# Kernel tuning notes

Hardware: AMD Instinct MI355X
Metric: run time of the kernel (lower is better)

Reference implementation:

```python
import jax, jax.numpy as jnp
import numpy as np
import math

N, S, D, H, L, F = 4, 2048, 512, 8, 4, 200
HD = D // H
EPS = 1e-5


def _pos_encoding(seq_len, d_model, dtype):
    pos = jnp.arange(seq_len, dtype=jnp.float32)[:, None]            # [S,1]
    div = jnp.exp(jnp.arange(0, d_model, 2, dtype=jnp.float32) * (-math.log(10000.0) / d_model))
    ang = pos * div                                                   # [S,D/2]
    pe = jnp.stack([jnp.sin(ang), jnp.cos(ang)], axis=-1).reshape(seq_len, d_model)
    return pe.astype(dtype)


def _layernorm(x, w, b):
    mu = jnp.mean(x, axis=-1, keepdims=True)
    var = jnp.mean(jnp.square(x - mu), axis=-1, keepdims=True)
    return (x - mu) * jax.lax.rsqrt(var + EPS) * w + b


def setup_inputs() -> dict:
    key = jax.random.key(0)
    ks = jax.random.split(key, 8)
    std = 0.02
    inp = {
        "features": jax.random.normal(ks[0], (N, S, D), dtype=jnp.float32),
        # attention projections, stored as [L, in, out] (math-equivalent to torch x @ W.T + b)
        "Wq": jax.random.normal(ks[1], (L, D, D), dtype=jnp.float32) * std,
        "bq": jnp.zeros((L, D), dtype=jnp.float32),
        "Wk": jax.random.normal(ks[2], (L, D, D), dtype=jnp.float32) * std,
        "bk": jnp.zeros((L, D), dtype=jnp.float32),
        "Wv": jax.random.normal(ks[3], (L, D, D), dtype=jnp.float32) * std,
        "bv": jnp.zeros((L, D), dtype=jnp.float32),
        "Wo": jax.random.normal(ks[4], (L, D, D), dtype=jnp.float32) * std,
        "bo": jnp.zeros((L, D), dtype=jnp.float32),
        # FFN
        "W1": jax.random.normal(ks[5], (L, D, F), dtype=jnp.float32) * std,
        "b1": jnp.zeros((L, F), dtype=jnp.float32),
        "W2": jax.random.normal(ks[6], (L, F, D), dtype=jnp.float32) * std,
        "b2": jnp.zeros((L, D), dtype=jnp.float32),
        # layernorms
        "ln1_w": jnp.ones((L, D), dtype=jnp.float32),
        "ln1_b": jnp.zeros((L, D), dtype=jnp.float32),
        "ln2_w": jnp.ones((L, D), dtype=jnp.float32),
        "ln2_b": jnp.zeros((L, D), dtype=jnp.float32),
    }
    return inp


def _encoder(features, Wq, bq, Wk, bk, Wv, bv, Wo, bo, W1, b1, W2, b2,
             ln1_w, ln1_b, ln2_w, ln2_b):
    n, s, d = features.shape
    x = features + _pos_encoding(s, d, features.dtype)[None]  # PositionalEncoding (dropout=identity in eval)
    scale = 1.0 / math.sqrt(HD)
    for l in range(L):
        # MultiHeadAttention: manual QK^T -> softmax -> AV
        q = (x @ Wq[l] + bq[l]).reshape(n, s, H, HD)
        k = (x @ Wk[l] + bk[l]).reshape(n, s, H, HD)
        v = (x @ Wv[l] + bv[l]).reshape(n, s, H, HD)
        attn = jnp.einsum("nshd,nthd->nhst", q, k) * scale          # [N,H,S,S]
        score = jax.nn.softmax(attn, axis=-1)
        y = jnp.einsum("nhst,nthd->nshd", score, v).reshape(n, s, d)
        attn_out = y @ Wo[l] + bo[l]
        x = _layernorm(x + attn_out, ln1_w[l], ln1_b[l])
        # FFN: linear2(relu(linear1(x)))
        ff = jax.nn.relu(x @ W1[l] + b1[l]) @ W2[l] + b2[l]
        x = _layernorm(x + ff, ln2_w[l], ln2_b[l])
    return x


def reference(features, Wq, bq, Wk, bk, Wv, bv, Wo, bo, W1, b1, W2, b2,
              ln1_w, ln1_b, ln2_w, ln2_b):
    return _encoder(features, Wq, bq, Wk, bk, Wv, bv, Wo, bo, W1, b1, W2, b2,
                    ln1_w, ln1_b, ln2_w, ln2_b)
```

## Files before the change

### kernel.cpp

```cpp
#include <hip/hip_runtime.h>
#include <hip/hip_bf16.h>
#include <cstdint>


typedef __bf16 bf16;
typedef __bf16 bf16x8 __attribute__((ext_vector_type(8)));
typedef float f32x4 __attribute__((ext_vector_type(4)));

#define MFMA16(a, b, c) __builtin_amdgcn_mfma_f32_16x16x32_bf16((a), (b), (c), 0, 0, 0)

static constexpr int NB   = 4;
static constexpr int SQ   = 2048;
static constexpr int DM   = 512;
static constexpr int NH   = 8;
static constexpr int HD   = 64;
static constexpr int NL   = 4;
static constexpr int FF   = 200;
static constexpr int FFP  = 256;
static constexpr int MTOK = NB * SQ;

__device__ __forceinline__ float fast_exp2(float x) {
#if __has_builtin(__builtin_amdgcn_exp2f)
    return __builtin_amdgcn_exp2f(x);
#else
    return exp2f(x);
#endif
}

__device__ __forceinline__ void gld16(bf16* l, const bf16* g) {
    __builtin_amdgcn_global_load_lds(
        (const __attribute__((address_space(1))) void*)g,
        (__attribute__((address_space(3))) void*)l, 16, 0, 0);
}

__global__ __launch_bounds__(256) void convw_kernel(
    const float* __restrict__ Wq, const float* __restrict__ Wk,
    const float* __restrict__ Wv, const float* __restrict__ Wo,
    const float* __restrict__ W1, const float* __restrict__ W2,
    bf16* __restrict__ wqkvt, bf16* __restrict__ wot,
    bf16* __restrict__ w1t, bf16* __restrict__ w2t)
{
    __shared__ float tile[32][33];
    const int z = blockIdx.z, l = z / 6, which = z % 6;
    const float* src; bf16* dst; int K, Nsrc, Npad, Kpad;
    switch (which) {
        case 0: src = Wq + (size_t)l*DM*DM; dst = wqkvt + (size_t)(l*3+0)*DM*DM; K=DM; Nsrc=DM; Npad=DM; Kpad=DM; break;
        case 1: src = Wk + (size_t)l*DM*DM; dst = wqkvt + (size_t)(l*3+1)*DM*DM; K=DM; Nsrc=DM; Npad=DM; Kpad=DM; break;
        case 2: src = Wv + (size_t)l*DM*DM; dst = wqkvt + (size_t)(l*3+2)*DM*DM; K=DM; Nsrc=DM; Npad=DM; Kpad=DM; break;
        case 3: src = Wo + (size_t)l*DM*DM; dst = wot   + (size_t)l*DM*DM;       K=DM; Nsrc=DM; Npad=DM; Kpad=DM; break;
        case 4: src = W1 + (size_t)l*DM*FF; dst = w1t   + (size_t)l*FFP*DM;      K=DM; Nsrc=FF; Npad=FFP; Kpad=DM; break;
        default:src = W2 + (size_t)l*FF*DM; dst = w2t   + (size_t)l*DM*FFP;      K=FF; Nsrc=DM; Npad=DM; Kpad=FFP; break;
    }
    const int k0 = blockIdx.x * 32, n0 = blockIdx.y * 32;
    if (k0 >= Kpad || n0 >= Npad) return;
    const int tr = threadIdx.x >> 3, tc = (threadIdx.x & 7) * 4;
    for (int c = 0; c < 4; c++) {
        int sr = k0 + tr, sc = n0 + tc + c;
        tile[tr][tc + c] = (sr < K && sc < Nsrc) ? src[(size_t)sr * Nsrc + sc] : 0.f;
    }
    __syncthreads();
    const int dr = n0 + tr;
    if (dr < Npad) {
        for (int c = 0; c < 4; c++) {
            int dc = k0 + tc + c;
            if (dc < Kpad) dst[(size_t)dr * Kpad + dc] = (bf16)tile[tc + c][tr];
        }
    }
}

__global__ __launch_bounds__(256) void posenc_kernel(
    const float* __restrict__ f, float* __restrict__ x, bf16* __restrict__ xb)
{
    const int t = blockIdx.x * 256 + threadIdx.x;
    const int d2 = t & 255, row = t >> 8, s = row & (SQ - 1);
    const float kfac = -0.03597789207803197f;
    float dv = __expf((float)d2 * kfac);
    float ang = (float)s * dv;
    float pe0 = sinf(ang), pe1 = cosf(ang);
    const size_t base = (size_t)row * DM + d2 * 2;
    float2 fv = *(const float2*)(f + base);
    float o0 = fv.x + pe0, o1 = fv.y + pe1;
    *(float2*)(x + base) = make_float2(o0, o1);
    union { bf16 h[2]; unsigned int u; } pk;
    pk.h[0] = (bf16)o0; pk.h[1] = (bf16)o1;
    *(unsigned int*)(xb + base) = pk.u;
}

__device__ __forceinline__ void gemm128_core(
    const bf16* __restrict__ A, const bf16* __restrict__ Wt, int K,
    int m0, int n0, bf16* As, bf16* Bs, f32x4 (&acc)[4][4])
{
    const int tid = threadIdx.x;
    const int w = tid >> 6, lane = tid & 63;
    const int l15 = lane & 15, quad = lane >> 4;
    const int srow = w * 16 + (lane >> 2);
    const int scol = (lane & 3) * 8;
    const bf16* Ag = A  + (size_t)(m0 + srow) * K + scol;
    const bf16* Bg = Wt + (size_t)(n0 + srow) * K + scol;
    bf16* AsW = As + w * 512;
    bf16* BsW = Bs + w * 512;
    const int wm = (w >> 1) * 64, wn = (w & 1) * 64;

    for (int k0 = 0; k0 < K; k0 += 32) {
        __syncthreads();
        gld16(AsW,        Ag + k0);
        gld16(AsW + 2048, Ag + (size_t)64 * K + k0);
        gld16(BsW,        Bg + k0);
        gld16(BsW + 2048, Bg + (size_t)64 * K + k0);
        asm volatile("s_waitcnt vmcnt(0)" ::: "memory");
        __syncthreads();

        bf16x8 af[4], bfr[4];
        #pragma unroll
        for (int i = 0; i < 4; i++)
            af[i] = *(const bf16x8*)&As[(wm + i * 16 + l15) * 32 + quad * 8];
        #pragma unroll
        for (int j = 0; j < 4; j++)
            bfr[j] = *(const bf16x8*)&Bs[(wn + j * 16 + l15) * 32 + quad * 8];
        #pragma unroll
        for (int i = 0; i < 4; i++)
            #pragma unroll
            for (int j = 0; j < 4; j++)
                acc[i][j] = MFMA16(af[i], bfr[j], acc[i][j]);
    }
}

__global__ __launch_bounds__(256, 2) void gemm128_kernel(
    const bf16* __restrict__ A, const bf16* __restrict__ Wt,
    const float* __restrict__ bias, int nbias,
    float* __restrict__ outf, bf16* __restrict__ outb,
    int K, int Nc, int mode)
{
    __shared__ alignas(16) bf16 As[128 * 32];
    __shared__ alignas(16) bf16 Bs[128 * 32];
    const int m0 = blockIdx.x * 128, n0 = blockIdx.y * 128;
    f32x4 acc[4][4] = {};
    gemm128_core(A, Wt, K, m0, n0, As, Bs, acc);

    const int lane = threadIdx.x & 63;
    const int l15 = lane & 15, quad = lane >> 4;
    const int w = threadIdx.x >> 6;
    const int wm = (w >> 1) * 64, wn = (w & 1) * 64;
    #pragma unroll
    for (int j = 0; j < 4; j++) {
        const int col = n0 + wn + j * 16 + l15;
        const float bv = (col < nbias) ? bias[col] : 0.f;
        #pragma unroll
        for (int i = 0; i < 4; i++) {
            const int rbase = m0 + wm + i * 16 + quad * 4;
            #pragma unroll
            for (int r = 0; r < 4; r++) {
                float v = acc[i][j][r] + bv;
                const int row = rbase + r;
                if (mode == 0)      outf[(size_t)row * Nc + col] = v;
                else if (mode == 1) outb[(size_t)row * Nc + col] = (bf16)v;
                else                outb[(size_t)row * Nc + col] = (bf16)fmaxf(v, 0.f);
            }
        }
    }
}

__global__ __launch_bounds__(256, 2) void gemm128_qkv_kernel(
    const bf16* __restrict__ xb, const bf16* __restrict__ Wt,
    const float* __restrict__ bq, const float* __restrict__ bk,
    const float* __restrict__ bv,
    bf16* __restrict__ qb, bf16* __restrict__ kb, bf16* __restrict__ vtb)
{
    __shared__ alignas(16) bf16 As[128 * 32];
    __shared__ alignas(16) bf16 Bs[128 * 32];
    const int m0 = blockIdx.x * 128, n0 = blockIdx.y * 128;
    f32x4 acc[4][4] = {};
    gemm128_core(xb, Wt, DM, m0, n0, As, Bs, acc);

    const int lane = threadIdx.x & 63;
    const int l15 = lane & 15, quad = lane >> 4;
    const int w = threadIdx.x >> 6;
    const int wm = (w >> 1) * 64, wn = (w & 1) * 64;
    const int which = n0 >> 9;
    const float* bias = (which == 0) ? bq : (which == 1) ? bk : bv;
    const float scale = (which == 0) ? 0.18033688f : 1.f;
    #pragma unroll
    for (int j = 0; j < 4; j++) {
        const int c = (n0 & 511) + wn + j * 16 + l15;
        const float bvv = bias[c];
        #pragma unroll
        for (int i = 0; i < 4; i++) {
            const int rbase = m0 + wm + i * 16 + quad * 4;
            #pragma unroll
            for (int r = 0; r < 4; r++) {
                float v = (acc[i][j][r] + bvv) * scale;
                const int row = rbase + r;
                if (which == 0)      qb[(size_t)row * DM + c] = (bf16)v;
                else if (which == 1) kb[(size_t)row * DM + c] = (bf16)v;
                else {
                    const int n = row >> 11, s = row & (SQ - 1);
                    const int h = c >> 6, hd = c & 63;
                    vtb[((size_t)(((n << 3) | h) << 6 | hd) << 11) | s] = (bf16)v;
                }
            }
        }
    }
}

__global__ __launch_bounds__(256, 2) void attn_kernel(
    const bf16* __restrict__ qb, const bf16* __restrict__ kb,
    const bf16* __restrict__ vtb, bf16* __restrict__ yb)
{
    __shared__ alignas(16) bf16 Kt[2][64][72];
    __shared__ alignas(16) bf16 Vt[2][64][72];
    __shared__ alignas(16) bf16 Pt[4][32][72];
    const int tid = threadIdx.x;
    const int w = tid >> 6, lane = tid & 63;
    const int l15 = lane & 15, quad = lane >> 4;
    const int id = blockIdx.x;
    const int nh = (id & 7) * 4 + ((id >> 3) & 3);
    const int qblk = id >> 5;
    const int n = nh >> 3, h = nh & 7;
    const int q0 = qblk * 128 + w * 32;
    const bf16* qbase = qb + (size_t)n * SQ * DM + h * HD;
    const bf16* kbase = kb + (size_t)n * SQ * DM + h * HD;
    const bf16* vbase = vtb + (size_t)nh * HD * SQ;

    bf16x8 qf[2][2];
    for (int mi = 0; mi < 2; mi++)
        for (int hh = 0; hh < 2; hh++)
            qf[mi][hh] = *(const bf16x8*)(qbase + (size_t)(q0 + mi*16 + l15) * DM + hh*32 + quad*8);

    f32x4 o[2][4] = {};
    float lsum[2] = {0.f, 0.f};

    const int srow = tid >> 2, seg = (tid & 3) * 16;
    const bf16* krow = kbase + (size_t)srow * DM + seg;
    const bf16* vrow = vbase + (size_t)srow * SQ + seg;

    {
        bf16x8 k0 = *(const bf16x8*)(krow);
        bf16x8 k1 = *(const bf16x8*)(krow + 8);
        bf16x8 v0 = *(const bf16x8*)(vrow);
        bf16x8 v1 = *(const bf16x8*)(vrow + 8);
        *(bf16x8*)&Kt[0][srow][seg]     = k0;
        *(bf16x8*)&Kt[0][srow][seg + 8] = k1;
        *(bf16x8*)&Vt[0][srow][seg]     = v0;
        *(bf16x8*)&Vt[0][srow][seg + 8] = v1;
    }

    for (int jt = 0; jt < SQ / 64; jt++) {
        const int buf = jt & 1;
        __syncthreads();
        const bool pre = (jt + 1 < SQ / 64);
        bf16x8 k0, k1, v0, v1;
        if (pre) {
            const bf16* kp = krow + (size_t)(jt + 1) * 64 * DM;
            const bf16* vp = vrow + (jt + 1) * 64;
            k0 = *(const bf16x8*)(kp);
            k1 = *(const bf16x8*)(kp + 8);
            v0 = *(const bf16x8*)(vp);
            v1 = *(const bf16x8*)(vp + 8);
        }

        bf16x8 kf[4][2];
        #pragma unroll
        for (int s4 = 0; s4 < 4; s4++) {
            kf[s4][0] = *(const bf16x8*)&Kt[buf][s4*16 + l15][quad*8];
            kf[s4][1] = *(const bf16x8*)&Kt[buf][s4*16 + l15][32 + quad*8];
        }
        #pragma unroll
        for (int mi = 0; mi < 2; mi++) {
            #pragma unroll
            for (int s4 = 0; s4 < 4; s4++) {
                f32x4 sacc = {};
                sacc = MFMA16(kf[s4][0], qf[mi][0], sacc);
                sacc = MFMA16(kf[s4][1], qf[mi][1], sacc);
                union { bf16 hh[4]; uint2 u; } pk;
                #pragma unroll
                for (int r = 0; r < 4; r++) {
                    float pv = fast_exp2(sacc[r]);
                    lsum[mi] += pv;
                    pk.hh[r] = (bf16)pv;
                }
                *(uint2*)&Pt[w][mi*16 + l15][s4*16 + quad*4] = pk.u;
            }
        }
        asm volatile("s_waitcnt lgkmcnt(0)" ::: "memory");

        bf16x8 pf[2][2];
        #pragma unroll
        for (int mi = 0; mi < 2; mi++) {
            pf[mi][0] = *(const bf16x8*)&Pt[w][mi*16 + l15][quad*8];
            pf[mi][1] = *(const bf16x8*)&Pt[w][mi*16 + l15][32 + quad*8];
        }
        #pragma unroll
        for (int d4 = 0; d4 < 4; d4++) {
            bf16x8 vv0 = *(const bf16x8*)&Vt[buf][d4*16 + l15][quad*8];
            bf16x8 vv1 = *(const bf16x8*)&Vt[buf][d4*16 + l15][32 + quad*8];
            #pragma unroll
            for (int mi = 0; mi < 2; mi++) {
                o[mi][d4] = MFMA16(pf[mi][0], vv0, o[mi][d4]);
                o[mi][d4] = MFMA16(pf[mi][1], vv1, o[mi][d4]);
            }
        }

        if (pre) {
            *(bf16x8*)&Kt[buf^1][srow][seg]     = k0;
            *(bf16x8*)&Kt[buf^1][srow][seg + 8] = k1;
            *(bf16x8*)&Vt[buf^1][srow][seg]     = v0;
            *(bf16x8*)&Vt[buf^1][srow][seg + 8] = v1;
        }
    }

    #pragma unroll
    for (int mi = 0; mi < 2; mi++) {
        lsum[mi] += __shfl_xor(lsum[mi], 16, 64);
        lsum[mi] += __shfl_xor(lsum[mi], 32, 64);
    }
    #pragma unroll
    for (int mi = 0; mi < 2; mi++) {
        f32x4 rl;
        #pragma unroll
        for (int r = 0; r < 4; r++)
            rl[r] = 1.f / __shfl(lsum[mi], quad * 4 + r, 64);
        #pragma unroll
        for (int d4 = 0; d4 < 4; d4++) {
            const int col = h * HD + d4 * 16 + l15;
            #pragma unroll
            for (int r = 0; r < 4; r++) {
                const int row = n * SQ + q0 + mi*16 + quad*4 + r;
                yb[(size_t)row * DM + col] = (bf16)(o[mi][d4][r] * rl[r]);
            }
        }
    }
}

__global__ __launch_bounds__(256) void ln_kernel(
    const float* __restrict__ res, const float* __restrict__ add,
    const float* __restrict__ g, const float* __restrict__ beta,
    float* __restrict__ outf, bf16* __restrict__ outb)
{
    const int w = threadIdx.x >> 6, lane = threadIdx.x & 63;
    const size_t row = (size_t)blockIdx.x * 4 + w;
    const float4* rp = (const float4*)(res + row * DM);
    const float4* ap = (const float4*)(add + row * DM);
    float4 v[2];
    float s = 0.f, s2 = 0.f;
    #pragma unroll
    for (int i = 0; i < 2; i++) {
        const int idx = i * 64 + lane;
        float4 a = rp[idx], c = ap[idx];
        float x0 = a.x + c.x, x1 = a.y + c.y, x2 = a.z + c.z, x3 = a.w + c.w;
        v[i] = make_float4(x0, x1, x2, x3);
        s  += x0 + x1 + x2 + x3;
        s2 += x0*x0 + x1*x1 + x2*x2 + x3*x3;
    }
    for (int m = 1; m < 64; m <<= 1) {
        s  += __shfl_xor(s,  m, 64);
        s2 += __shfl_xor(s2, m, 64);
    }
    const float mean = s * (1.f / DM);
    const float var  = s2 * (1.f / DM) - mean * mean;
    const float rstd = rsqrtf(var + 1e-5f);
    #pragma unroll
    for (int i = 0; i < 2; i++) {
        const int idx = i * 64 + lane;
        float4 gw = ((const float4*)g)[idx], bw = ((const float4*)beta)[idx];
        float o0 = (v[i].x - mean) * rstd * gw.x + bw.x;
        float o1 = (v[i].y - mean) * rstd * gw.y + bw.y;
        float o2 = (v[i].z - mean) * rstd * gw.z + bw.z;
        float o3 = (v[i].w - mean) * rstd * gw.w + bw.w;
        ((float4*)(outf + row * DM))[idx] = make_float4(o0, o1, o2, o3);
        union { bf16 h[4]; uint2 u; } pk;
        pk.h[0] = (bf16)o0; pk.h[1] = (bf16)o1; pk.h[2] = (bf16)o2; pk.h[3] = (bf16)o3;
        *(uint2*)(outb + row * DM + idx * 4) = pk.u;
    }
}

extern "C" void kernel_launch(void* const* d_in, const int* in_sizes, int n_in,
                              void* d_out, int out_size, void* d_ws, size_t ws_size,
                              hipStream_t stream)
{
    const float* features = (const float*)d_in[0];
    const float* Wq  = (const float*)d_in[1];
    const float* bq  = (const float*)d_in[2];
    const float* Wk  = (const float*)d_in[3];
    const float* bk  = (const float*)d_in[4];
    const float* Wv  = (const float*)d_in[5];
    const float* bv  = (const float*)d_in[6];
    const float* Wo  = (const float*)d_in[7];
    const float* bo  = (const float*)d_in[8];
    const float* W1  = (const float*)d_in[9];
    const float* b1  = (const float*)d_in[10];
    const float* W2  = (const float*)d_in[11];
    const float* b2  = (const float*)d_in[12];
    const float* ln1w = (const float*)d_in[13];
    const float* ln1b = (const float*)d_in[14];
    const float* ln2w = (const float*)d_in[15];
    const float* ln2b = (const float*)d_in[16];
    float* outp = (float*)d_out;

    char* p = (char*)d_ws;
    size_t off = 0;
    auto alloc = [&](size_t bytes) { void* r = p + off; off = (off + bytes + 255) & ~(size_t)255; return r; };
    const size_t tokD = (size_t)MTOK * DM;
    float* x     = (float*)alloc(tokD * 4);
    float* tmp   = (float*)alloc(tokD * 4);
    bf16* xb     = (bf16*)alloc(tokD * 2);
    bf16* qb     = (bf16*)alloc(tokD * 2);
    bf16* kb     = (bf16*)alloc(tokD * 2);
    bf16* vtb    = (bf16*)alloc(tokD * 2);
    bf16* yb     = (bf16*)alloc(tokD * 2);
    bf16* ffh    = (bf16*)alloc((size_t)MTOK * FFP * 2);
    bf16* wqkvt  = (bf16*)alloc((size_t)NL * 3 * DM * DM * 2);
    bf16* wot    = (bf16*)alloc((size_t)NL * DM * DM * 2);
    bf16* w1t    = (bf16*)alloc((size_t)NL * FFP * DM * 2);
    bf16* w2t    = (bf16*)alloc((size_t)NL * DM * FFP * 2);
    (void)ws_size; (void)in_sizes; (void)n_in; (void)out_size;

    convw_kernel<<<dim3(16, 16, NL * 6), 256, 0, stream>>>(
        Wq, Wk, Wv, Wo, W1, W2, wqkvt, wot, w1t, w2t);

    posenc_kernel<<<MTOK, 256, 0, stream>>>(features, x, xb);

    for (int l = 0; l < NL; l++) {
        const bf16* wqkvt_l = wqkvt + (size_t)l * 3 * DM * DM;
        gemm128_qkv_kernel<<<dim3(MTOK / 128, 1536 / 128), 256, 0, stream>>>(
            xb, wqkvt_l, bq + l*DM, bk + l*DM, bv + l*DM, qb, kb, vtb);
        attn_kernel<<<512, 256, 0, stream>>>(qb, kb, vtb, yb);
        gemm128_kernel<<<dim3(MTOK / 128, DM / 128), 256, 0, stream>>>(
            yb, wot + (size_t)l*DM*DM, bo + l*DM, DM, tmp, nullptr, DM, DM, 0);
        ln_kernel<<<MTOK / 4, 256, 0, stream>>>(x, tmp, ln1w + l*DM, ln1b + l*DM, x, xb);
        gemm128_kernel<<<dim3(MTOK / 128, FFP / 128), 256, 0, stream>>>(
            xb, w1t + (size_t)l*FFP*DM, b1 + l*FF, FF, nullptr, ffh, DM, FFP, 2);
        gemm128_kernel<<<dim3(MTOK / 128, DM / 128), 256, 0, stream>>>(
            ffh, w2t + (size_t)l*DM*FFP, b2 + l*DM, DM, tmp, nullptr, FFP, DM, 0);
        float* outdst = (l == NL - 1) ? outp : x;
        ln_kernel<<<MTOK / 4, 256, 0, stream>>>(x, tmp, ln2w + l*DM, ln2b + l*DM, outdst, xb);
    }
}
```

Baseline: 683.2 us.

## Keep attention probabilities in registers and fuse residual add into GEMM epilogue

```diff
diff --git a/kernel.cpp b/kernel.cpp
--- a/kernel.cpp
+++ b/kernel.cpp
@@ -5,9 +5,22 @@
 
 typedef __bf16 bf16;
 typedef __bf16 bf16x8 __attribute__((ext_vector_type(8)));
+typedef __bf16 bf16x4 __attribute__((ext_vector_type(4)));
+typedef short short4v __attribute__((ext_vector_type(4)));
 typedef float f32x4 __attribute__((ext_vector_type(4)));
 
 #define MFMA16(a, b, c) __builtin_amdgcn_mfma_f32_16x16x32_bf16((a), (b), (c), 0, 0, 0)
+
+__device__ __forceinline__ f32x4 mfma_k16(bf16x4 a, bf16x4 b, f32x4 c) {
+#if __has_builtin(__builtin_amdgcn_mfma_f32_16x16x16_bf16)
+    return __builtin_amdgcn_mfma_f32_16x16x16_bf16(a, b, c, 0, 0, 0);
+#else
+    short4v as, bs;
+    __builtin_memcpy(&as, &a, 8);
+    __builtin_memcpy(&bs, &b, 8);
+    return __builtin_amdgcn_mfma_f32_16x16x16bf16_1k(as, bs, c, 0, 0, 0);
+#endif
+}
 
 static constexpr int NB   = 4;
 static constexpr int SQ   = 2048;
@@ -128,6 +141,7 @@
 __global__ __launch_bounds__(256, 2) void gemm128_kernel(
     const bf16* __restrict__ A, const bf16* __restrict__ Wt,
     const float* __restrict__ bias, int nbias,
+    const float* __restrict__ resid,
     float* __restrict__ outf, bf16* __restrict__ outb,
     int K, int Nc, int mode)
 {
@@ -152,9 +166,10 @@
             for (int r = 0; r < 4; r++) {
                 float v = acc[i][j][r] + bv;
                 const int row = rbase + r;
-                if (mode == 0)      outf[(size_t)row * Nc + col] = v;
-                else if (mode == 1) outb[(size_t)row * Nc + col] = (bf16)v;
-                else                outb[(size_t)row * Nc + col] = (bf16)fmaxf(v, 0.f);
+                const size_t idx = (size_t)row * Nc + col;
+                if (mode == 0)      outf[idx] = v + (resid ? resid[idx] : 0.f);
+                else if (mode == 1) outb[idx] = (bf16)v;
+                else                outb[idx] = (bf16)fmaxf(v, 0.f);
             }
         }
     }
@@ -207,8 +222,7 @@
     const bf16* __restrict__ vtb, bf16* __restrict__ yb)
 {
     __shared__ alignas(16) bf16 Kt[2][64][72];
-    __shared__ alignas(16) bf16 Vt[2][64][72];
-    __shared__ alignas(16) bf16 Pt[4][32][72];
+    __shared__ alignas(16) bf16 Vt[2 * 64 * 68];
     const int tid = threadIdx.x;
     const int w = tid >> 6, lane = tid & 63;
     const int l15 = lane & 15, quad = lane >> 4;
@@ -233,6 +247,17 @@
     const bf16* krow = kbase + (size_t)srow * DM + seg;
     const bf16* vrow = vbase + (size_t)srow * SQ + seg;
 
+    auto storeV = [&](int buf, bf16x8 a, bf16x8 b) {
+        bf16* d = &Vt[(buf * 64 + srow) * 68 + seg];
+        bf16x4 p0, p1, p2, p3;
+        #pragma unroll
+        for (int i = 0; i < 4; i++) { p0[i]=a[i]; p1[i]=a[i+4]; p2[i]=b[i]; p3[i]=b[i+4]; }
+        *(bf16x4*)(d)      = p0;
+        *(bf16x4*)(d + 4)  = p1;
+        *(bf16x4*)(d + 8)  = p2;
+        *(bf16x4*)(d + 12) = p3;
+    };
+
     {
         bf16x8 k0 = *(const bf16x8*)(krow);
         bf16x8 k1 = *(const bf16x8*)(krow + 8);
@@ -240,8 +265,7 @@
         bf16x8 v1 = *(const bf16x8*)(vrow + 8);
         *(bf16x8*)&Kt[0][srow][seg]     = k0;
         *(bf16x8*)&Kt[0][srow][seg + 8] = k1;
-        *(bf16x8*)&Vt[0][srow][seg]     = v0;
-        *(bf16x8*)&Vt[0][srow][seg + 8] = v1;
+        storeV(0, v0, v1);
     }
 
     for (int jt = 0; jt < SQ / 64; jt++) {
@@ -258,53 +282,38 @@
             v1 = *(const bf16x8*)(vp + 8);
         }
 
-        bf16x8 kf[4][2];
         #pragma unroll
         for (int s4 = 0; s4 < 4; s4++) {
-            kf[s4][0] = *(const bf16x8*)&Kt[buf][s4*16 + l15][quad*8];
-            kf[s4][1] = *(const bf16x8*)&Kt[buf][s4*16 + l15][32 + quad*8];
-        }
-        #pragma unroll
-        for (int mi = 0; mi < 2; mi++) {
-            #pragma unroll
-            for (int s4 = 0; s4 < 4; s4++) {
+            bf16x8 kf0 = *(const bf16x8*)&Kt[buf][s4*16 + l15][quad*8];
+            bf16x8 kf1 = *(const bf16x8*)&Kt[buf][s4*16 + l15][32 + quad*8];
+            bf16x4 pf[2];
+            #pragma unroll
+            for (int mi = 0; mi < 2; mi++) {
                 f32x4 sacc = {};
-                sacc = MFMA16(kf[s4][0], qf[mi][0], sacc);
-                sacc = MFMA16(kf[s4][1], qf[mi][1], sacc);
-                union { bf16 hh[4]; uint2 u; } pk;
-                #pragma unroll
-                for (int r = 0; r < 4; r++) {
-                    float pv = fast_exp2(sacc[r]);
-                    lsum[mi] += pv;
-                    pk.hh[r] = (bf16)pv;
-                }
-                *(uint2*)&Pt[w][mi*16 + l15][s4*16 + quad*4] = pk.u;
+                sacc = MFMA16(kf0, qf[mi][0], sacc);
+                sacc = MFMA16(kf1, qf[mi][1], sacc);
+                float p0 = fast_exp2(sacc[0]);
+                float p1 = fast_exp2(sacc[1]);
+                float p2 = fast_exp2(sacc[2]);
+                float p3 = fast_exp2(sacc[3]);
+                lsum[mi] += (p0 + p1) + (p2 + p3);
+                bf16x4 pk;
+                pk[0] = (bf16)p0; pk[1] = (bf16)p1;
+                pk[2] = (bf16)p2; pk[3] = (bf16)p3;
+                pf[mi] = pk;
             }
-        }
-        asm volatile("s_waitcnt lgkmcnt(0)" ::: "memory");
-
-        bf16x8 pf[2][2];
-        #pragma unroll
-        for (int mi = 0; mi < 2; mi++) {
-            pf[mi][0] = *(const bf16x8*)&Pt[w][mi*16 + l15][quad*8];
-            pf[mi][1] = *(const bf16x8*)&Pt[w][mi*16 + l15][32 + quad*8];
-        }
-        #pragma unroll
-        for (int d4 = 0; d4 < 4; d4++) {
-            bf16x8 vv0 = *(const bf16x8*)&Vt[buf][d4*16 + l15][quad*8];
-            bf16x8 vv1 = *(const bf16x8*)&Vt[buf][d4*16 + l15][32 + quad*8];
-            #pragma unroll
-            for (int mi = 0; mi < 2; mi++) {
-                o[mi][d4] = MFMA16(pf[mi][0], vv0, o[mi][d4]);
-                o[mi][d4] = MFMA16(pf[mi][1], vv1, o[mi][d4]);
+            #pragma unroll
+            for (int d4 = 0; d4 < 4; d4++) {
+                bf16x4 vf = *(const bf16x4*)&Vt[(buf*64 + d4*16 + l15) * 68 + s4*16 + quad*4];
+                o[0][d4] = mfma_k16(pf[0], vf, o[0][d4]);
+                o[1][d4] = mfma_k16(pf[1], vf, o[1][d4]);
             }
         }
 
         if (pre) {
             *(bf16x8*)&Kt[buf^1][srow][seg]     = k0;
             *(bf16x8*)&Kt[buf^1][srow][seg + 8] = k1;
-            *(bf16x8*)&Vt[buf^1][srow][seg]     = v0;
-            *(bf16x8*)&Vt[buf^1][srow][seg + 8] = v1;
+            storeV(buf^1, v0, v1);
         }
     }
 
@@ -332,24 +341,22 @@
 }
 
 __global__ __launch_bounds__(256) void ln_kernel(
-    const float* __restrict__ res, const float* __restrict__ add,
+    const float* __restrict__ xin,
     const float* __restrict__ g, const float* __restrict__ beta,
     float* __restrict__ outf, bf16* __restrict__ outb)
 {
     const int w = threadIdx.x >> 6, lane = threadIdx.x & 63;
     const size_t row = (size_t)blockIdx.x * 4 + w;
-    const float4* rp = (const float4*)(res + row * DM);
-    const float4* ap = (const float4*)(add + row * DM);
+    const float4* rp = (const float4*)(xin + row * DM);
     float4 v[2];
     float s = 0.f, s2 = 0.f;
     #pragma unroll
     for (int i = 0; i < 2; i++) {
         const int idx = i * 64 + lane;
-        float4 a = rp[idx], c = ap[idx];
-        float x0 = a.x + c.x, x1 = a.y + c.y, x2 = a.z + c.z, x3 = a.w + c.w;
-        v[i] = make_float4(x0, x1, x2, x3);
-        s  += x0 + x1 + x2 + x3;
-        s2 += x0*x0 + x1*x1 + x2*x2 + x3*x3;
+        float4 a = rp[idx];
+        v[i] = a;
+        s  += a.x + a.y + a.z + a.w;
+        s2 += a.x*a.x + a.y*a.y + a.z*a.z + a.w*a.w;
     }
     for (int m = 1; m < 64; m <<= 1) {
         s  += __shfl_xor(s,  m, 64);
@@ -425,13 +432,13 @@
             xb, wqkvt_l, bq + l*DM, bk + l*DM, bv + l*DM, qb, kb, vtb);
         attn_kernel<<<512, 256, 0, stream>>>(qb, kb, vtb, yb);
         gemm128_kernel<<<dim3(MTOK / 128, DM / 128), 256, 0, stream>>>(
-            yb, wot + (size_t)l*DM*DM, bo + l*DM, DM, tmp, nullptr, DM, DM, 0);
-        ln_kernel<<<MTOK / 4, 256, 0, stream>>>(x, tmp, ln1w + l*DM, ln1b + l*DM, x, xb);
+            yb, wot + (size_t)l*DM*DM, bo + l*DM, DM, x, tmp, nullptr, DM, DM, 0);
+        ln_kernel<<<MTOK / 4, 256, 0, stream>>>(tmp, ln1w + l*DM, ln1b + l*DM, x, xb);
         gemm128_kernel<<<dim3(MTOK / 128, FFP / 128), 256, 0, stream>>>(
-            xb, w1t + (size_t)l*FFP*DM, b1 + l*FF, FF, nullptr, ffh, DM, FFP, 2);
+            xb, w1t + (size_t)l*FFP*DM, b1 + l*FF, FF, nullptr, nullptr, ffh, DM, FFP, 2);
         gemm128_kernel<<<dim3(MTOK / 128, DM / 128), 256, 0, stream>>>(
-            ffh, w2t + (size_t)l*DM*FFP, b2 + l*DM, DM, tmp, nullptr, FFP, DM, 0);
+            ffh, w2t + (size_t)l*DM*FFP, b2 + l*DM, DM, x, tmp, nullptr, FFP, DM, 0);
         float* outdst = (l == NL - 1) ? outp : x;
-        ln_kernel<<<MTOK / 4, 256, 0, stream>>>(x, tmp, ln2w + l*DM, ln2b + l*DM, outdst, xb);
-    }
-}
+        ln_kernel<<<MTOK / 4, 256, 0, stream>>>(tmp, ln2w + l*DM, ln2b + l*DM, outdst, xb);
+    }
+}
```

Result: slower. 750.6 us (+9.9%).
